# Optimization experiments

Measured on AMD Instinct MI355X. Metric: run time of the kernel, lower is better.

Reference implementation:

```python
import jax, jax.numpy as jnp
import numpy as np
from jax import lax

B, V, K, E = 32768, 256, 4, 2048
INTERVENTION_STRENGTH = 1.0
PROP_SCALE = 0.1
N_ROUNDS = 3


def setup_inputs() -> dict:
    key = jax.random.key(0)
    ks = jax.random.split(key, 20)
    s = 0.02
    return {
        "original_data": jax.random.normal(ks[0], (B, V), jnp.float32),
        "intervention_values": jax.random.normal(ks[1], (B, K), jnp.float32),
        "strengths": jax.random.uniform(ks[2], (E,), jnp.float32),
        "intervention_variables": jnp.arange(K, dtype=jnp.int32),
        "cause_idx": jax.random.randint(ks[3], (E,), 0, V, jnp.int32),
        "effect_idx": jax.random.randint(ks[4], (E,), 0, V, jnp.int32),
        # per-intervention-variable estimator MLPs: Linear(V,64) -> ReLU -> Linear(64,V)
        "est_W1": jax.random.normal(ks[5], (K, 64, V), jnp.float32) * s,
        "est_b1": jnp.zeros((K, 64), jnp.float32),
        "est_W2": jax.random.normal(ks[6], (K, V, 64), jnp.float32) * s,
        "est_b2": jnp.zeros((K, V), jnp.float32),
        # plausibility scorer: Linear(3V,128) -> ReLU -> Linear(128,64) -> ReLU -> Linear(64,1) -> Sigmoid
        "pl_W1": jax.random.normal(ks[7], (128, 3 * V), jnp.float32) * s,
        "pl_b1": jnp.zeros((128,), jnp.float32),
        "pl_W2": jax.random.normal(ks[8], (64, 128), jnp.float32) * s,
        "pl_b2": jnp.zeros((64,), jnp.float32),
        "pl_W3": jax.random.normal(ks[9], (1, 64), jnp.float32) * s,
        "pl_b3": jnp.zeros((1,), jnp.float32),
    }


def _propagate(data, cause_idx, effect_idx, strengths):
    # Faithful sequential in-place edge updates (effect of edge k may feed edge k+1).
    def step(d, ces):
        c, e, st = ces
        infl = d[:, c] * (st * PROP_SCALE)  # [B]
        return d.at[:, e].add(infl), None

    def round_body(d, _):
        d, _ = lax.scan(step, d, (cause_idx, effect_idx, strengths))
        return d, None

    d, _ = lax.scan(round_body, data, None, length=N_ROUNDS)
    return d


def reference(original_data, intervention_values, strengths,
              est_W1, est_b1, est_W2, est_b2,
              pl_W1, pl_b1, pl_W2, pl_b2, pl_W3, pl_b3,
              intervention_variables, cause_idx, effect_idx):
    x = original_data  # [B, V]
    ivars = intervention_variables  # [K] int, constant

    # do-intervention: overwrite selected columns
    intervened = x.at[:, ivars].set(intervention_values)  # [B, V]

    # intervention effect estimators, vectorized over the K intervened variables
    h = jax.nn.relu(jnp.einsum('bv,kov->bko', x, est_W1) + est_b1)          # [B, K, 64]
    eff = jnp.einsum('bko,kvo->bkv', h, est_W2) + est_b2                     # [B, K, V]
    mag = jnp.abs(intervention_values - x[:, ivars])                         # [B, K]
    intervention_effects = jnp.einsum('bkv,bk->bv', eff, mag) * INTERVENTION_STRENGTH  # [B, V]

    # sequential causal propagation over edge list, 3 rounds
    final_cf = _propagate(intervened + intervention_effects, cause_idx, effect_idx, strengths)

    # plausibility scorer MLP
    pin = jnp.concatenate([x, intervened, final_cf], axis=1)                 # [B, 3V]
    p = jax.nn.relu(pin @ pl_W1.T + pl_b1)
    p = jax.nn.relu(p @ pl_W2.T + pl_b2)
    plaus = jax.nn.sigmoid(p @ pl_W3.T + pl_b3)                              # [B, 1]

    impact = jnp.linalg.norm(final_cf - x, axis=1, keepdims=True)            # [B, 1]
    return final_cf, intervention_effects, plaus, impact
```

## Files before the change

kernel.cpp:

```cpp
#include <hip/hip_runtime.h>

#define BDIM 32768
#define VDIM 256
#define KVAR 4
#define EDIM 2048
#define SEGS 16
#define SEGLEN 128

typedef __attribute__((ext_vector_type(8))) short short8;
typedef __attribute__((ext_vector_type(4))) float f32x4;

__device__ __forceinline__ unsigned short f2b(float f){
  union { float f; unsigned u; } v; v.f = f;
  unsigned r = v.u + 0x7FFFu + ((v.u >> 16) & 1u);
  return (unsigned short)(r >> 16);
}
__device__ __forceinline__ float b2f(unsigned short h){
  union { unsigned u; float f; } v; v.u = ((unsigned)h) << 16;
  return v.f;
}
__device__ __forceinline__ short8 ldb8(const unsigned short* p){
  return *(const short8*)p;
}

__device__ __forceinline__ void gl_lds16(const unsigned short* g, unsigned short* l){
  __builtin_amdgcn_global_load_lds(
      (const __attribute__((address_space(1))) unsigned int*)g,
      (__attribute__((address_space(3))) unsigned int*)l, 16, 0, 0);
}

__device__ __forceinline__ void stage256(const unsigned short* Bt, int kB,
                                         int w, int lane, unsigned short* Bs){
#pragma unroll
  for (int i = 0; i < 4; i++){
    int g8 = i*8 + w;
    int r  = g8*8 + (lane >> 3);
    int s  = lane & 7;
    gl_lds16(Bt + (size_t)r*VDIM + kB + ((s ^ (r & 7)) << 3),
             Bs + (size_t)g8*512);
  }
}
__device__ __forceinline__ void stage128(const unsigned short* Bt, int kB,
                                         int w, int lane, unsigned short* Bs){
#pragma unroll
  for (int i = 0; i < 2; i++){
    int g8 = i*8 + w;
    int r  = g8*8 + (lane >> 3);
    int s  = lane & 7;
    gl_lds16(Bt + (size_t)r*VDIM + kB + ((s ^ (r & 7)) << 3),
             Bs + (size_t)g8*512);
  }
}
__device__ __forceinline__ void stageA64(const unsigned short* XBg, int rowBlk,
                                         int w, int lane, unsigned short* As){
#pragma unroll
  for (int i = 0; i < 4; i++){
    int pair = i*8 + w;
    int r = pair*2 + (lane >> 5);
    int s = lane & 31;
    gl_lds16(XBg + (size_t)(rowBlk + r)*VDIM + ((s ^ (r & 7)) << 3),
             As + (size_t)pair*512);
  }
}

__device__ __forceinline__ short8 bs_frag(const unsigned short* Bs, int c, int klocal){
  int slot = klocal >> 3;
  return *(const short8*)&Bs[(size_t)c*64 + ((slot ^ (c & 7)) << 3)];
}

template<int NF>
__device__ __forceinline__ void mm_lA(const unsigned short* Alds,
                                      const unsigned short* Bs,
                                      int rl0, int c0, int kb, int kB,
                                      f32x4 (&acc)[2][NF])
{
  int sw = (rl0 & 7) << 3;
#pragma unroll
  for (int k = 0; k < 2; k++){
    int ka = kB + k*32 + kb;
    short8 a0 = *(const short8*)&Alds[(size_t)rl0 * 256 + (ka ^ sw)];
    short8 a1 = *(const short8*)&Alds[(size_t)(rl0+16) * 256 + (ka ^ sw)];
#pragma unroll
    for (int fn = 0; fn < NF; fn++){
      short8 b = bs_frag(Bs, c0 + fn*16, k*32 + kb);
      acc[0][fn] = __builtin_amdgcn_mfma_f32_16x16x32_bf16(a0, b, acc[0][fn], 0, 0, 0);
      acc[1][fn] = __builtin_amdgcn_mfma_f32_16x16x32_bf16(a1, b, acc[1][fn], 0, 0, 0);
    }
  }
}
template<int NF, int KSZ>
__device__ __forceinline__ void mm_l1(const unsigned short* Alds, int ldaE,
                                      const unsigned short* Bt, int ldb,
                                      int rl0, int c0, int kb,
                                      f32x4 (&acc)[NF])
{
  int sw = (rl0 & 7) << 3;
#pragma unroll
  for (int k0 = 0; k0 < KSZ; k0 += 32){
    int ka = k0 + kb;
    short8 a0 = *(const short8*)&Alds[(size_t)rl0 * ldaE + (ka ^ sw)];
#pragma unroll
    for (int fn = 0; fn < NF; fn++){
      short8 b = ldb8(Bt + (size_t)(c0 + fn*16)*ldb + ka);
      acc[fn] = __builtin_amdgcn_mfma_f32_16x16x32_bf16(a0, b, acc[fn], 0, 0, 0);
    }
  }
}

__global__ __launch_bounds__(256) void prep_seg(
    const float* X, const float* IV, const int* ivars,
    const float* eW1, const float* eW2, const float* pW1, const float* pW2,
    const int* cidx, const int* eidx, const float* stren,
    unsigned short* XB,
    unsigned short* bt1, unsigned short* bt2,
    unsigned short* w1ab, unsigned short* w1c,
    unsigned short* w2bf, float* w1bcol, int* colmap,
    float* delta, float* segs)
{
  if (blockIdx.x < 1024){
    __shared__ int lc[SEGLEN];
    __shared__ int le[SEGLEN];
    __shared__ float la[SEGLEN];
    int bid = blockIdx.x;
    int seg = bid >> 6;
    int rowbase = (bid & 63) * 4;
    int w = threadIdx.x >> 6, lane = threadIdx.x & 63;
    int row = rowbase + w;
    int k0 = seg * SEGLEN;
    for (int t = threadIdx.x; t < SEGLEN; t += 256){
      lc[t] = cidx[k0 + t]; le[t] = eidx[k0 + t]; la[t] = stren[k0 + t] * 0.1f;
    }
    __syncthreads();
    float r0 = (row == lane)        ? 1.f : 0.f;
    float r1 = (row == lane + 64)   ? 1.f : 0.f;
    float r2 = (row == lane + 128)  ? 1.f : 0.f;
    float r3 = (row == lane + 192)  ? 1.f : 0.f;
    for (int t = 0; t < SEGLEN; t++){
      int cs = __builtin_amdgcn_readfirstlane(lc[t]);
      int es = __builtin_amdgcn_readfirstlane(le[t]);
      float a = la[t];
      float vr;
      switch (cs >> 6){ case 0: vr = r0; break; case 1: vr = r1; break;
                        case 2: vr = r2; break; default: vr = r3; }
      float v = __shfl(vr, cs & 63, 64);
      float add = (lane == (es & 63)) ? a * v : 0.f;
      switch (es >> 6){ case 0: r0 += add; break; case 1: r1 += add; break;
                        case 2: r2 += add; break; default: r3 += add; }
    }
    float* out = segs + (size_t)seg * 65536 + (size_t)row * 256;
    out[lane] = r0; out[lane + 64] = r1; out[lane + 128] = r2; out[lane + 192] = r3;
    return;
  }
  int stride = 1024 * 256;
  int g0 = (blockIdx.x - 1024) * 256 + threadIdx.x;
  for (int i = g0; i < (BDIM * VDIM) / 8; i += stride){
    const float* p = X + (size_t)i * 8;
    f32x4 lo = *(const f32x4*)p;
    f32x4 hi = *(const f32x4*)(p + 4);
    short8 r;
    r[0]=(short)f2b(lo[0]); r[1]=(short)f2b(lo[1]); r[2]=(short)f2b(lo[2]); r[3]=(short)f2b(lo[3]);
    r[4]=(short)f2b(hi[0]); r[5]=(short)f2b(hi[1]); r[6]=(short)f2b(hi[2]); r[7]=(short)f2b(hi[3]);
    *(short8*)(XB + (size_t)i * 8) = r;
  }
  for (int i = g0; i < 65536; i += stride) bt1[i] = f2b(eW1[i]);
  for (int i = g0; i < 65536; i += stride){
    int v = i >> 8, r = i & 255;
    bt2[i] = f2b(eW2[(r >> 6) * 16384 + v * 64 + (r & 63)]);
  }
  for (int i = g0; i < 32768; i += stride){
    int o = i >> 8, v = i & 255;
    w1ab[i] = f2b(pW1[o*768 + v] + pW1[o*768 + 256 + v]);
    w1c[i]  = f2b(pW1[o*768 + 512 + v]);
  }
  for (int i = g0; i < 8192; i += stride) w2bf[i] = f2b(pW2[i]);
  for (int i = g0; i < 512; i += stride){
    int o = i >> 2, k = i & 3;
    w1bcol[i] = pW1[o*768 + 256 + ivars[k]];
  }
  for (int i = g0; i < VDIM; i += stride){
    int m = -1;
#pragma unroll
    for (int k = 0; k < KVAR; k++) if (ivars[k] == i) m = k;
    colmap[i] = m;
  }
  for (int i = g0; i < BDIM * KVAR; i += stride){
    int b = i >> 2, k = i & 3;
    delta[i] = IV[i] - X[(size_t)b * VDIM + ivars[k]];
  }
}

__global__ __launch_bounds__(256) void combine4(const float* S, float* Out)
{
  int m = blockIdx.x >> 6;
  int rb = (blockIdx.x & 63) * 4;
  int c = threadIdx.x;
  __shared__ float v[4][256];
  const float* base = S + (size_t)m * 4 * 65536;
#pragma unroll
  for (int r = 0; r < 4; r++) v[r][c] = base[(size_t)(rb + r) * 256 + c];
  __syncthreads();
  for (int p = 1; p < 4; p++){
    const float* Bm = base + (size_t)p * 65536;
    float a0 = 0.f, a1 = 0.f, a2 = 0.f, a3 = 0.f;
    for (int k = 0; k < 256; k += 4){
      f32x4 v0 = *(const f32x4*)&v[0][k];
      f32x4 v1 = *(const f32x4*)&v[1][k];
      f32x4 v2 = *(const f32x4*)&v[2][k];
      f32x4 v3 = *(const f32x4*)&v[3][k];
#pragma unroll
      for (int j = 0; j < 4; j++){
        float bk = Bm[(size_t)(k + j) * 256 + c];
        a0 += v0[j] * bk; a1 += v1[j] * bk; a2 += v2[j] * bk; a3 += v3[j] * bk;
      }
    }
    __syncthreads();
    v[0][c] = a0; v[1][c] = a1; v[2][c] = a2; v[3][c] = a3;
    __syncthreads();
  }
#pragma unroll
  for (int r = 0; r < 4; r++) Out[(size_t)m * 65536 + (size_t)(rb + r) * 256 + c] = v[r][c];
}

__global__ __launch_bounds__(256) void powM(const float* R, unsigned short* Mt)
{
  int rb = blockIdx.x * 4;
  int c = threadIdx.x;
  __shared__ float v[4][256];
#pragma unroll
  for (int r = 0; r < 4; r++) v[r][c] = R[(size_t)(rb + r) * 256 + c];
  __syncthreads();
  for (int p = 0; p < 2; p++){
    float a0 = 0.f, a1 = 0.f, a2 = 0.f, a3 = 0.f;
    for (int k = 0; k < 256; k += 4){
      f32x4 v0 = *(const f32x4*)&v[0][k];
      f32x4 v1 = *(const f32x4*)&v[1][k];
      f32x4 v2 = *(const f32x4*)&v[2][k];
      f32x4 v3 = *(const f32x4*)&v[3][k];
#pragma unroll
      for (int j = 0; j < 4; j++){
        float bk = R[(size_t)(k + j) * 256 + c];
        a0 += v0[j] * bk; a1 += v1[j] * bk; a2 += v2[j] * bk; a3 += v3[j] * bk;
      }
    }
    __syncthreads();
    v[0][c] = a0; v[1][c] = a1; v[2][c] = a2; v[3][c] = a3;
    __syncthreads();
  }
#pragma unroll
  for (int r = 0; r < 4; r++) Mt[(size_t)c * 256 + (rb + r)] = f2b(v[r][c]);
}

__global__ __launch_bounds__(512) void mega3(
    const float* IV, const unsigned short* XB,
    const unsigned short* Bt1, const unsigned short* Bt2, const unsigned short* Mt,
    const unsigned short* W1ab, const unsigned short* W1c, const unsigned short* W2bf,
    const float* eb1, const float* eb2, const float* delta, const int* colmap,
    const float* w1bcol, const float* pb1, const float* pb2,
    const float* W3, const float* pb3,
    float* effOut, float* outF, float* plausOut, float* impOut)
{
  __shared__ unsigned short xbs[64 * 256];
  __shared__ unsigned short buf[64 * 256];
  __shared__ unsigned short Bs0[256 * 64];
  __shared__ unsigned short Bs1[256 * 64];
  __shared__ float impLds[64 * 4];
  int tid = threadIdx.x, w = tid >> 6, lane = tid & 63;
  int rowg = w >> 2, colg = w & 3;
  int rowBlk = blockIdx.x * 64;
  int rl0 = rowg * 32 + (lane & 15);
  int colBase = colg * 64;
  int c0 = colBase + (lane & 15);
  int kb = (lane >> 4) * 8;
  f32x4 acc[2][4];

  auto stage_unit = [&](int u, unsigned short* Bs){
    if (u < 4)       stage256(Bt1, u*64, w, lane, Bs);
    else if (u < 8)  stage256(Bt2, (u-4)*64, w, lane, Bs);
    else if (u < 12) stage256(Mt, (u-8)*64, w, lane, Bs);
    else           { stage128(W1ab, (u-12)*64, w, lane, Bs);
                     stage128(W1c,  (u-12)*64, w, lane, Bs + 8192); }
  };

  stageA64(XB, rowBlk, w, lane, xbs);
  stage_unit(0, Bs0);
  __syncthreads();

#pragma unroll
  for (int fm = 0; fm < 2; fm++)
#pragma unroll
    for (int fn = 0; fn < 4; fn++) acc[fm][fn] = (f32x4){0.f,0.f,0.f,0.f};
#pragma unroll
  for (int kc = 0; kc < 4; kc++){
    int u = kc;
    stage_unit(u + 1, (u & 1) ? Bs0 : Bs1);
    __builtin_amdgcn_s_setprio(1);
    mm_lA<4>(xbs, (u & 1) ? Bs1 : Bs0, rl0, c0, kb, kc*64, acc);
    __builtin_amdgcn_s_setprio(0);
    __syncthreads();
  }
  {
    float b1v[4];
#pragma unroll
    for (int fn = 0; fn < 4; fn++) b1v[fn] = eb1[colBase + fn*16 + (lane & 15)];
#pragma unroll
    for (int fm = 0; fm < 2; fm++)
#pragma unroll
      for (int i = 0; i < 4; i++){
        int rl = rowg*32 + fm*16 + (lane >> 4)*4 + i;
        int gr = rowBlk + rl;
        float mg = fabsf(delta[gr*4 + colg]);
        int sw = (rl & 7) << 3;
#pragma unroll
        for (int fn = 0; fn < 4; fn++){
          int col = colBase + fn*16 + (lane & 15);
          float h = acc[fm][fn][i] + b1v[fn];
          h = h > 0.f ? h : 0.f;
          buf[(size_t)rl*256 + (col ^ sw)] = f2b(h * mg);
        }
      }
  }
  __syncthreads();

#pragma unroll
  for (int fm = 0; fm < 2; fm++)
#pragma unroll
    for (int fn = 0; fn < 4; fn++) acc[fm][fn] = (f32x4){0.f,0.f,0.f,0.f};
#pragma unroll
  for (int kc = 0; kc < 4; kc++){
    int u = 4 + kc;
    stage_unit(u + 1, (u & 1) ? Bs0 : Bs1);
    __builtin_amdgcn_s_setprio(1);
    mm_lA<4>(buf, (u & 1) ? Bs1 : Bs0, rl0, c0, kb, kc*64, acc);
    __builtin_amdgcn_s_setprio(0);
    __syncthreads();
  }
  {
    float bb0[4], bb1[4], bb2[4], bb3[4];
    int imv[4];
#pragma unroll
    for (int fn = 0; fn < 4; fn++){
      int col = colBase + fn*16 + (lane & 15);
      bb0[fn] = eb2[col]; bb1[fn] = eb2[256 + col];
      bb2[fn] = eb2[512 + col]; bb3[fn] = eb2[768 + col];
      imv[fn] = colmap[col];
    }
#pragma unroll
    for (int fm = 0; fm < 2; fm++)
#pragma unroll
      for (int i = 0; i < 4; i++){
        int rl = rowg*32 + fm*16 + (lane >> 4)*4 + i;
        int gr = rowBlk + rl;
        f32x4 dl = *(const f32x4*)&delta[gr*4];
        float d0a = fabsf(dl[0]), d1a = fabsf(dl[1]), d2a = fabsf(dl[2]), d3a = fabsf(dl[3]);
        int sw = (rl & 7) << 3;
#pragma unroll
        for (int fn = 0; fn < 4; fn++){
          int col = colBase + fn*16 + (lane & 15);
          float eff = acc[fm][fn][i] + d0a*bb0[fn] + d1a*bb1[fn] + d2a*bb2[fn] + d3a*bb3[fn];
          size_t idx = (size_t)gr*VDIM + col;
          effOut[idx] = eff;
          float base = (imv[fn] >= 0) ? IV[gr*4 + imv[fn]]
                                      : b2f(xbs[(size_t)rl*256 + (col ^ sw)]);
          buf[(size_t)rl*256 + (col ^ sw)] = f2b(base + eff);
        }
      }
  }
  __syncthreads();

#pragma unroll
  for (int fm = 0; fm < 2; fm++)
#pragma unroll
    for (int fn = 0; fn < 4; fn++) acc[fm][fn] = (f32x4){0.f,0.f,0.f,0.f};
#pragma unroll
  for (int kc = 0; kc < 4; kc++){
    int u = 8 + kc;
    stage_unit(u + 1, (u & 1) ? Bs0 : Bs1);
    __builtin_amdgcn_s_setprio(1);
    mm_lA<4>(buf, (u & 1) ? Bs1 : Bs0, rl0, c0, kb, kc*64, acc);
    __builtin_amdgcn_s_setprio(0);
    __syncthreads();
  }
  {
#pragma unroll
    for (int fm = 0; fm < 2; fm++)
#pragma unroll
      for (int i = 0; i < 4; i++){
        int rl = rowg*32 + fm*16 + (lane >> 4)*4 + i;
        int gr = rowBlk + rl;
        int sw = (rl & 7) << 3;
        float ss = 0.f;
#pragma unroll
        for (int fn = 0; fn < 4; fn++){
          int col = colBase + fn*16 + (lane & 15);
          size_t idx = (size_t)gr*VDIM + col;
          float fv = acc[fm][fn][i];
          outF[idx] = fv;
          buf[(size_t)rl*256 + (col ^ sw)] = f2b(fv);
          float d = fv - b2f(xbs[(size_t)rl*256 + (col ^ sw)]);
          ss += d * d;
        }
        ss += __shfl_xor(ss, 1, 64); ss += __shfl_xor(ss, 2, 64);
        ss += __shfl_xor(ss, 4, 64); ss += __shfl_xor(ss, 8, 64);
        if ((lane & 15) == 0) impLds[rl*4 + colg] = ss;
      }
  }
  __syncthreads();

  {
    f32x4 a4[2][2];
#pragma unroll
    for (int fm = 0; fm < 2; fm++)
#pragma unroll
      for (int fn = 0; fn < 2; fn++) a4[fm][fn] = (f32x4){0.f,0.f,0.f,0.f};
    int c4 = colg * 32 + (lane & 15);
#pragma unroll
    for (int kc = 0; kc < 4; kc++){
      int u = 12 + kc;
      if (kc < 3) stage_unit(u + 1, (u & 1) ? Bs0 : Bs1);
      const unsigned short* B = (u & 1) ? Bs1 : Bs0;
      __builtin_amdgcn_s_setprio(1);
      mm_lA<2>(xbs, B, rl0, c4, kb, kc*64, a4);
      mm_lA<2>(buf, B + 8192, rl0, c4, kb, kc*64, a4);
      __builtin_amdgcn_s_setprio(0);
      __syncthreads();
    }
    float bv[2];
    f32x4 wb[2];
#pragma unroll
    for (int fn = 0; fn < 2; fn++){
      int col = colg*32 + fn*16 + (lane & 15);
      bv[fn] = pb1[col];
      wb[fn] = *(const f32x4*)&w1bcol[col*4];
    }
#pragma unroll
    for (int fm = 0; fm < 2; fm++)
#pragma unroll
      for (int i = 0; i < 4; i++){
        int rl = rowg*32 + fm*16 + (lane >> 4)*4 + i;
        int gr = rowBlk + rl;
        f32x4 dl = *(const f32x4*)&delta[gr*4];
        int sw = (rl & 7) << 3;
#pragma unroll
        for (int fn = 0; fn < 2; fn++){
          int col = colg*32 + fn*16 + (lane & 15);
          float p = a4[fm][fn][i] + bv[fn]
                  + dl[0]*wb[fn][0] + dl[1]*wb[fn][1] + dl[2]*wb[fn][2] + dl[3]*wb[fn][3];
          p = p > 0.f ? p : 0.f;
          buf[(size_t)rl*128 + (col ^ sw)] = f2b(p);
        }
      }
  }
  __syncthreads();

  if (w < 4){
    int rl0b = w * 16 + (lane & 15);
    f32x4 a2[4];
#pragma unroll
    for (int fn = 0; fn < 4; fn++) a2[fn] = (f32x4){0.f,0.f,0.f,0.f};
    mm_l1<4, 128>(buf, 128, W2bf, 128, rl0b, (lane & 15), kb, a2);
    float b2v[4], w3v[4];
#pragma unroll
    for (int fn = 0; fn < 4; fn++){
      int col = fn*16 + (lane & 15);
      b2v[fn] = pb2[col]; w3v[fn] = W3[col];
    }
    float b3v = pb3[0];
#pragma unroll
    for (int i = 0; i < 4; i++){
      float s = 0.f;
#pragma unroll
      for (int fn = 0; fn < 4; fn++){
        float p2 = a2[fn][i] + b2v[fn];
        p2 = p2 > 0.f ? p2 : 0.f;
        s += p2 * w3v[fn];
      }
      s += __shfl_xor(s, 1, 64); s += __shfl_xor(s, 2, 64);
      s += __shfl_xor(s, 4, 64); s += __shfl_xor(s, 8, 64);
      if ((lane & 15) == 0){
        int gr = rowBlk + w*16 + (lane >> 4)*4 + i;
        plausOut[gr] = 1.f / (1.f + expf(-(s + b3v)));
      }
    }
  } else if (w == 4){
    f32x4 v = *(const f32x4*)&impLds[lane * 4];
    impOut[rowBlk + lane] = sqrtf(v[0] + v[1] + v[2] + v[3]);
  }
}

#define WS_XB     ((size_t)0)
#define WS_DELTA  ((size_t)16777216)
#define WS_SEG    ((size_t)17301504)
#define WS_T2     ((size_t)21495808)
#define WS_R      ((size_t)22544384)
#define WS_MT     ((size_t)22806528)
#define WS_BT1    ((size_t)22937600)
#define WS_BT2    ((size_t)23068672)
#define WS_W1AB   ((size_t)23199744)
#define WS_W1C    ((size_t)23265280)
#define WS_W2BF   ((size_t)23330816)
#define WS_W1BCOL ((size_t)23347200)
#define WS_COLMAP ((size_t)23349248)

extern "C" void kernel_launch(void* const* d_in, const int* in_sizes, int n_in,
                              void* d_out, int out_size, void* d_ws, size_t ws_size,
                              hipStream_t stream)
{
  const float* X     = (const float*)d_in[0];
  const float* IV    = (const float*)d_in[1];
  const float* STR   = (const float*)d_in[2];
  const int*   IVARS = (const int*)d_in[3];
  const int*   CIDX  = (const int*)d_in[4];
  const int*   EIDX  = (const int*)d_in[5];
  const float* EW1   = (const float*)d_in[6];
  const float* EB1   = (const float*)d_in[7];
  const float* EW2   = (const float*)d_in[8];
  const float* EB2   = (const float*)d_in[9];
  const float* PW1   = (const float*)d_in[10];
  const float* PB1   = (const float*)d_in[11];
  const float* PW2   = (const float*)d_in[12];
  const float* PB2   = (const float*)d_in[13];
  const float* PW3   = (const float*)d_in[14];
  const float* PB3   = (const float*)d_in[15];

  char* ws = (char*)d_ws;
  unsigned short* XB     = (unsigned short*)(ws + WS_XB);
  float*          DELTA  = (float*)(ws + WS_DELTA);
  float*          SEG    = (float*)(ws + WS_SEG);
  float*          T2     = (float*)(ws + WS_T2);
  float*          Rm     = (float*)(ws + WS_R);
  unsigned short* MT     = (unsigned short*)(ws + WS_MT);
  unsigned short* BT1    = (unsigned short*)(ws + WS_BT1);
  unsigned short* BT2    = (unsigned short*)(ws + WS_BT2);
  unsigned short* W1AB   = (unsigned short*)(ws + WS_W1AB);
  unsigned short* W1C    = (unsigned short*)(ws + WS_W1C);
  unsigned short* W2BF   = (unsigned short*)(ws + WS_W2BF);
  float*          W1BCOL = (float*)(ws + WS_W1BCOL);
  int*            COLMAP = (int*)(ws + WS_COLMAP);

  float* outF   = (float*)d_out;
  float* outEff = outF + (size_t)BDIM * VDIM;
  float* outPl  = outEff + (size_t)BDIM * VDIM;
  float* outIm  = outPl + BDIM;

  prep_seg<<<2048, 256, 0, stream>>>(X, IV, IVARS, EW1, EW2, PW1, PW2,
                                     CIDX, EIDX, STR,
                                     XB, BT1, BT2, W1AB, W1C, W2BF, W1BCOL, COLMAP,
                                     DELTA, SEG);
  combine4<<<256, 256, 0, stream>>>(SEG, T2);
  combine4<<<64, 256, 0, stream>>>(T2, Rm);
  powM<<<64, 256, 0, stream>>>(Rm, MT);

  mega3<<<512, 512, 0, stream>>>(IV, XB, BT1, BT2, MT, W1AB, W1C, W2BF,
                                 EB1, EB2, DELTA, COLMAP, W1BCOL,
                                 PB1, PB2, PW3, PB3,
                                 outEff, outF, outPl, outIm);

  (void)in_sizes; (void)n_in; (void)out_size; (void)ws_size;
}
```

Measured before the change: 167.6 us.

## Double waves per block in fused kernel and widen matrix-combine grids

```diff
diff --git a/kernel.cpp b/kernel.cpp
--- a/kernel.cpp
+++ b/kernel.cpp
@@ -32,8 +32,8 @@
 __device__ __forceinline__ void stage256(const unsigned short* Bt, int kB,
                                          int w, int lane, unsigned short* Bs){
 #pragma unroll
-  for (int i = 0; i < 4; i++){
-    int g8 = i*8 + w;
+  for (int i = 0; i < 2; i++){
+    int g8 = i*16 + w;
     int r  = g8*8 + (lane >> 3);
     int s  = lane & 7;
     gl_lds16(Bt + (size_t)r*VDIM + kB + ((s ^ (r & 7)) << 3),
@@ -42,20 +42,17 @@
 }
 __device__ __forceinline__ void stage128(const unsigned short* Bt, int kB,
                                          int w, int lane, unsigned short* Bs){
-#pragma unroll
-  for (int i = 0; i < 2; i++){
-    int g8 = i*8 + w;
-    int r  = g8*8 + (lane >> 3);
-    int s  = lane & 7;
-    gl_lds16(Bt + (size_t)r*VDIM + kB + ((s ^ (r & 7)) << 3),
-             Bs + (size_t)g8*512);
-  }
+  int g8 = w;
+  int r  = g8*8 + (lane >> 3);
+  int s  = lane & 7;
+  gl_lds16(Bt + (size_t)r*VDIM + kB + ((s ^ (r & 7)) << 3),
+           Bs + (size_t)g8*512);
 }
 __device__ __forceinline__ void stageA64(const unsigned short* XBg, int rowBlk,
                                          int w, int lane, unsigned short* As){
 #pragma unroll
-  for (int i = 0; i < 4; i++){
-    int pair = i*8 + w;
+  for (int i = 0; i < 2; i++){
+    int pair = i*16 + w;
     int r = pair*2 + (lane >> 5);
     int s = lane & 31;
     gl_lds16(XBg + (size_t)(rowBlk + r)*VDIM + ((s ^ (r & 7)) << 3),
@@ -189,68 +186,52 @@
   }
 }
 
-__global__ __launch_bounds__(256) void combine4(const float* S, float* Out)
-{
-  int m = blockIdx.x >> 6;
-  int rb = (blockIdx.x & 63) * 4;
+__global__ __launch_bounds__(256) void combine4w(const float* S, float* Out)
+{
+  int m = blockIdx.x >> 8;
+  int r = blockIdx.x & 255;
   int c = threadIdx.x;
-  __shared__ float v[4][256];
+  __shared__ float v[256];
   const float* base = S + (size_t)m * 4 * 65536;
-#pragma unroll
-  for (int r = 0; r < 4; r++) v[r][c] = base[(size_t)(rb + r) * 256 + c];
+  v[c] = base[(size_t)r * 256 + c];
   __syncthreads();
   for (int p = 1; p < 4; p++){
     const float* Bm = base + (size_t)p * 65536;
-    float a0 = 0.f, a1 = 0.f, a2 = 0.f, a3 = 0.f;
-    for (int k = 0; k < 256; k += 4){
-      f32x4 v0 = *(const f32x4*)&v[0][k];
-      f32x4 v1 = *(const f32x4*)&v[1][k];
-      f32x4 v2 = *(const f32x4*)&v[2][k];
-      f32x4 v3 = *(const f32x4*)&v[3][k];
-#pragma unroll
-      for (int j = 0; j < 4; j++){
-        float bk = Bm[(size_t)(k + j) * 256 + c];
-        a0 += v0[j] * bk; a1 += v1[j] * bk; a2 += v2[j] * bk; a3 += v3[j] * bk;
-      }
-    }
-    __syncthreads();
-    v[0][c] = a0; v[1][c] = a1; v[2][c] = a2; v[3][c] = a3;
-    __syncthreads();
-  }
-#pragma unroll
-  for (int r = 0; r < 4; r++) Out[(size_t)m * 65536 + (size_t)(rb + r) * 256 + c] = v[r][c];
-}
-
-__global__ __launch_bounds__(256) void powM(const float* R, unsigned short* Mt)
-{
-  int rb = blockIdx.x * 4;
+    float a = 0.f;
+    for (int k = 0; k < 256; k += 8){
+#pragma unroll
+      for (int j = 0; j < 8; j++)
+        a += v[k + j] * Bm[(size_t)(k + j) * 256 + c];
+    }
+    __syncthreads();
+    v[c] = a;
+    __syncthreads();
+  }
+  Out[(size_t)m * 65536 + (size_t)r * 256 + c] = v[c];
+}
+
+__global__ __launch_bounds__(256) void powMw(const float* R, unsigned short* Mt)
+{
+  int r = blockIdx.x;
   int c = threadIdx.x;
-  __shared__ float v[4][256];
-#pragma unroll
-  for (int r = 0; r < 4; r++) v[r][c] = R[(size_t)(rb + r) * 256 + c];
+  __shared__ float v[256];
+  v[c] = R[(size_t)r * 256 + c];
   __syncthreads();
   for (int p = 0; p < 2; p++){
-    float a0 = 0.f, a1 = 0.f, a2 = 0.f, a3 = 0.f;
-    for (int k = 0; k < 256; k += 4){
-      f32x4 v0 = *(const f32x4*)&v[0][k];
-      f32x4 v1 = *(const f32x4*)&v[1][k];
-      f32x4 v2 = *(const f32x4*)&v[2][k];
-      f32x4 v3 = *(const f32x4*)&v[3][k];
-#pragma unroll
-      for (int j = 0; j < 4; j++){
-        float bk = R[(size_t)(k + j) * 256 + c];
-        a0 += v0[j] * bk; a1 += v1[j] * bk; a2 += v2[j] * bk; a3 += v3[j] * bk;
-      }
-    }
-    __syncthreads();
-    v[0][c] = a0; v[1][c] = a1; v[2][c] = a2; v[3][c] = a3;
-    __syncthreads();
-  }
-#pragma unroll
-  for (int r = 0; r < 4; r++) Mt[(size_t)c * 256 + (rb + r)] = f2b(v[r][c]);
-}
-
-__global__ __launch_bounds__(512) void mega3(
+    float a = 0.f;
+    for (int k = 0; k < 256; k += 8){
+#pragma unroll
+      for (int j = 0; j < 8; j++)
+        a += v[k + j] * R[(size_t)(k + j) * 256 + c];
+    }
+    __syncthreads();
+    v[c] = a;
+    __syncthreads();
+  }
+  Mt[(size_t)c * 256 + r] = f2b(v[c]);
+}
+
+__global__ __launch_bounds__(1024) void mega3(
     const float* IV, const unsigned short* XB,
     const unsigned short* Bt1, const unsigned short* Bt2, const unsigned short* Mt,
     const unsigned short* W1ab, const unsigned short* W1c, const unsigned short* W2bf,
@@ -263,15 +244,15 @@
   __shared__ unsigned short buf[64 * 256];
   __shared__ unsigned short Bs0[256 * 64];
   __shared__ unsigned short Bs1[256 * 64];
-  __shared__ float impLds[64 * 4];
+  __shared__ float impLds[64 * 8];
   int tid = threadIdx.x, w = tid >> 6, lane = tid & 63;
-  int rowg = w >> 2, colg = w & 3;
+  int rowg = w >> 3, colg = w & 7;
   int rowBlk = blockIdx.x * 64;
   int rl0 = rowg * 32 + (lane & 15);
-  int colBase = colg * 64;
+  int colBase = colg * 32;
   int c0 = colBase + (lane & 15);
   int kb = (lane >> 4) * 8;
-  f32x4 acc[2][4];
+  f32x4 acc[2][2];
 
   auto stage_unit = [&](int u, unsigned short* Bs){
     if (u < 4)       stage256(Bt1, u*64, w, lane, Bs);
@@ -288,30 +269,31 @@
 #pragma unroll
   for (int fm = 0; fm < 2; fm++)
 #pragma unroll
-    for (int fn = 0; fn < 4; fn++) acc[fm][fn] = (f32x4){0.f,0.f,0.f,0.f};
+    for (int fn = 0; fn < 2; fn++) acc[fm][fn] = (f32x4){0.f,0.f,0.f,0.f};
 #pragma unroll
   for (int kc = 0; kc < 4; kc++){
     int u = kc;
     stage_unit(u + 1, (u & 1) ? Bs0 : Bs1);
     __builtin_amdgcn_s_setprio(1);
-    mm_lA<4>(xbs, (u & 1) ? Bs1 : Bs0, rl0, c0, kb, kc*64, acc);
+    mm_lA<2>(xbs, (u & 1) ? Bs1 : Bs0, rl0, c0, kb, kc*64, acc);
     __builtin_amdgcn_s_setprio(0);
     __syncthreads();
   }
   {
-    float b1v[4];
-#pragma unroll
-    for (int fn = 0; fn < 4; fn++) b1v[fn] = eb1[colBase + fn*16 + (lane & 15)];
+    float b1v[2];
+#pragma unroll
+    for (int fn = 0; fn < 2; fn++) b1v[fn] = eb1[colBase + fn*16 + (lane & 15)];
+    int kI = colg >> 1;
 #pragma unroll
     for (int fm = 0; fm < 2; fm++)
 #pragma unroll
       for (int i = 0; i < 4; i++){
         int rl = rowg*32 + fm*16 + (lane >> 4)*4 + i;
         int gr = rowBlk + rl;
-        float mg = fabsf(delta[gr*4 + colg]);
+        float mg = fabsf(delta[gr*4 + kI]);
         int sw = (rl & 7) << 3;
 #pragma unroll
-        for (int fn = 0; fn < 4; fn++){
+        for (int fn = 0; fn < 2; fn++){
           int col = colBase + fn*16 + (lane & 15);
           float h = acc[fm][fn][i] + b1v[fn];
           h = h > 0.f ? h : 0.f;
@@ -324,21 +306,21 @@
 #pragma unroll
   for (int fm = 0; fm < 2; fm++)
 #pragma unroll
-    for (int fn = 0; fn < 4; fn++) acc[fm][fn] = (f32x4){0.f,0.f,0.f,0.f};
+    for (int fn = 0; fn < 2; fn++) acc[fm][fn] = (f32x4){0.f,0.f,0.f,0.f};
 #pragma unroll
   for (int kc = 0; kc < 4; kc++){
     int u = 4 + kc;
     stage_unit(u + 1, (u & 1) ? Bs0 : Bs1);
     __builtin_amdgcn_s_setprio(1);
-    mm_lA<4>(buf, (u & 1) ? Bs1 : Bs0, rl0, c0, kb, kc*64, acc);
+    mm_lA<2>(buf, (u & 1) ? Bs1 : Bs0, rl0, c0, kb, kc*64, acc);
     __builtin_amdgcn_s_setprio(0);
     __syncthreads();
   }
   {
-    float bb0[4], bb1[4], bb2[4], bb3[4];
-    int imv[4];
-#pragma unroll
-    for (int fn = 0; fn < 4; fn++){
+    float bb0[2], bb1[2], bb2[2], bb3[2];
+    int imv[2];
+#pragma unroll
+    for (int fn = 0; fn < 2; fn++){
       int col = colBase + fn*16 + (lane & 15);
       bb0[fn] = eb2[col]; bb1[fn] = eb2[256 + col];
       bb2[fn] = eb2[512 + col]; bb3[fn] = eb2[768 + col];
@@ -354,7 +336,7 @@
         float d0a = fabsf(dl[0]), d1a = fabsf(dl[1]), d2a = fabsf(dl[2]), d3a = fabsf(dl[3]);
         int sw = (rl & 7) << 3;
 #pragma unroll
-        for (int fn = 0; fn < 4; fn++){
+        for (int fn = 0; fn < 2; fn++){
           int col = colBase + fn*16 + (lane & 15);
           float eff = acc[fm][fn][i] + d0a*bb0[fn] + d1a*bb1[fn] + d2a*bb2[fn] + d3a*bb3[fn];
           size_t idx = (size_t)gr*VDIM + col;
@@ -370,13 +352,13 @@
 #pragma unroll
   for (int fm = 0; fm < 2; fm++)
 #pragma unroll
-    for (int fn = 0; fn < 4; fn++) acc[fm][fn] = (f32x4){0.f,0.f,0.f,0.f};
+    for (int fn = 0; fn < 2; fn++) acc[fm][fn] = (f32x4){0.f,0.f,0.f,0.f};
 #pragma unroll
   for (int kc = 0; kc < 4; kc++){
     int u = 8 + kc;
     stage_unit(u + 1, (u & 1) ? Bs0 : Bs1);
     __builtin_amdgcn_s_setprio(1);
-    mm_lA<4>(buf, (u & 1) ? Bs1 : Bs0, rl0, c0, kb, kc*64, acc);
+    mm_lA<2>(buf, (u & 1) ? Bs1 : Bs0, rl0, c0, kb, kc*64, acc);
     __builtin_amdgcn_s_setprio(0);
     __syncthreads();
   }
@@ -390,7 +372,7 @@
         int sw = (rl & 7) << 3;
         float ss = 0.f;
 #pragma unroll
-        for (int fn = 0; fn < 4; fn++){
+        for (int fn = 0; fn < 2; fn++){
           int col = colBase + fn*16 + (lane & 15);
           size_t idx = (size_t)gr*VDIM + col;
           float fv = acc[fm][fn][i];
@@ -401,37 +383,29 @@
         }
         ss += __shfl_xor(ss, 1, 64); ss += __shfl_xor(ss, 2, 64);
         ss += __shfl_xor(ss, 4, 64); ss += __shfl_xor(ss, 8, 64);
-        if ((lane & 15) == 0) impLds[rl*4 + colg] = ss;
+        if ((lane & 15) == 0) impLds[rl*8 + colg] = ss;
       }
   }
   __syncthreads();
 
   {
-    f32x4 a4[2][2];
-#pragma unroll
-    for (int fm = 0; fm < 2; fm++)
-#pragma unroll
-      for (int fn = 0; fn < 2; fn++) a4[fm][fn] = (f32x4){0.f,0.f,0.f,0.f};
-    int c4 = colg * 32 + (lane & 15);
+    f32x4 a4[2][1];
+#pragma unroll
+    for (int fm = 0; fm < 2; fm++) a4[fm][0] = (f32x4){0.f,0.f,0.f,0.f};
+    int c4 = colg*16 + (lane & 15);
 #pragma unroll
     for (int kc = 0; kc < 4; kc++){
       int u = 12 + kc;
       if (kc < 3) stage_unit(u + 1, (u & 1) ? Bs0 : Bs1);
       const unsigned short* B = (u & 1) ? Bs1 : Bs0;
       __builtin_amdgcn_s_setprio(1);
-      mm_lA<2>(xbs, B, rl0, c4, kb, kc*64, a4);
-      mm_lA<2>(buf, B + 8192, rl0, c4, kb, kc*64, a4);
+      mm_lA<1>(xbs, B, rl0, c4, kb, kc*64, a4);
+      mm_lA<1>(buf, B + 8192, rl0, c4, kb, kc*64, a4);
       __builtin_amdgcn_s_setprio(0);
       __syncthreads();
     }
-    float bv[2];
-    f32x4 wb[2];
-#pragma unroll
-    for (int fn = 0; fn < 2; fn++){
-      int col = colg*32 + fn*16 + (lane & 15);
-      bv[fn] = pb1[col];
-      wb[fn] = *(const f32x4*)&w1bcol[col*4];
-    }
+    float bv = pb1[c4];
+    f32x4 wb = *(const f32x4*)&w1bcol[c4*4];
 #pragma unroll
     for (int fm = 0; fm < 2; fm++)
 #pragma unroll
@@ -440,14 +414,10 @@
         int gr = rowBlk + rl;
         f32x4 dl = *(const f32x4*)&delta[gr*4];
         int sw = (rl & 7) << 3;
-#pragma unroll
-        for (int fn = 0; fn < 2; fn++){
-          int col = colg*32 + fn*16 + (lane & 15);
-          float p = a4[fm][fn][i] + bv[fn]
-                  + dl[0]*wb[fn][0] + dl[1]*wb[fn][1] + dl[2]*wb[fn][2] + dl[3]*wb[fn][3];
-          p = p > 0.f ? p : 0.f;
-          buf[(size_t)rl*128 + (col ^ sw)] = f2b(p);
-        }
+        float p = a4[fm][0][i] + bv
+                + dl[0]*wb[0] + dl[1]*wb[1] + dl[2]*wb[2] + dl[3]*wb[3];
+        p = p > 0.f ? p : 0.f;
+        buf[(size_t)rl*128 + (c4 ^ sw)] = f2b(p);
       }
   }
   __syncthreads();
@@ -482,8 +452,9 @@
       }
     }
   } else if (w == 4){
-    f32x4 v = *(const f32x4*)&impLds[lane * 4];
-    impOut[rowBlk + lane] = sqrtf(v[0] + v[1] + v[2] + v[3]);
+    f32x4 v0 = *(const f32x4*)&impLds[lane * 8];
+    f32x4 v1 = *(const f32x4*)&impLds[lane * 8 + 4];
+    impOut[rowBlk + lane] = sqrtf(v0[0]+v0[1]+v0[2]+v0[3]+v1[0]+v1[1]+v1[2]+v1[3]);
   }
 }
 
@@ -546,14 +517,14 @@
                                      CIDX, EIDX, STR,
                                      XB, BT1, BT2, W1AB, W1C, W2BF, W1BCOL, COLMAP,
                                      DELTA, SEG);
-  combine4<<<256, 256, 0, stream>>>(SEG, T2);
-  combine4<<<64, 256, 0, stream>>>(T2, Rm);
-  powM<<<64, 256, 0, stream>>>(Rm, MT);
-
-  mega3<<<512, 512, 0, stream>>>(IV, XB, BT1, BT2, MT, W1AB, W1C, W2BF,
-                                 EB1, EB2, DELTA, COLMAP, W1BCOL,
-                                 PB1, PB2, PW3, PB3,
-                                 outEff, outF, outPl, outIm);
+  combine4w<<<1024, 256, 0, stream>>>(SEG, T2);
+  combine4w<<<256, 256, 0, stream>>>(T2, Rm);
+  powMw<<<256, 256, 0, stream>>>(Rm, MT);
+
+  mega3<<<512, 1024, 0, stream>>>(IV, XB, BT1, BT2, MT, W1AB, W1C, W2BF,
+                                  EB1, EB2, DELTA, COLMAP, W1BCOL,
+                                  PB1, PB2, PW3, PB3,
+                                  outEff, outF, outPl, outIm);
 
   (void)in_sizes; (void)n_in; (void)out_size; (void)ws_size;
 }
```

New measurement: 247.6 us. +47.7%, slower.

## Move activation tiles from LDS to global scratch to cut shared memory use

Applied to the files above, without the earlier changes.

```diff
diff --git a/kernel.cpp b/kernel.cpp
--- a/kernel.cpp
+++ b/kernel.cpp
@@ -51,17 +51,6 @@
              Bs + (size_t)g8*512);
   }
 }
-__device__ __forceinline__ void stageA64(const unsigned short* XBg, int rowBlk,
-                                         int w, int lane, unsigned short* As){
-#pragma unroll
-  for (int i = 0; i < 4; i++){
-    int pair = i*8 + w;
-    int r = pair*2 + (lane >> 5);
-    int s = lane & 31;
-    gl_lds16(XBg + (size_t)(rowBlk + r)*VDIM + ((s ^ (r & 7)) << 3),
-             As + (size_t)pair*512);
-  }
-}
 
 __device__ __forceinline__ short8 bs_frag(const unsigned short* Bs, int c, int klocal){
   int slot = klocal >> 3;
@@ -69,17 +58,16 @@
 }
 
 template<int NF>
-__device__ __forceinline__ void mm_lA(const unsigned short* Alds,
+__device__ __forceinline__ void mm_gA(const unsigned short* A, int lda, int r0,
                                       const unsigned short* Bs,
-                                      int rl0, int c0, int kb, int kB,
+                                      int c0, int kb, int kB,
                                       f32x4 (&acc)[2][NF])
 {
-  int sw = (rl0 & 7) << 3;
 #pragma unroll
   for (int k = 0; k < 2; k++){
     int ka = kB + k*32 + kb;
-    short8 a0 = *(const short8*)&Alds[(size_t)rl0 * 256 + (ka ^ sw)];
-    short8 a1 = *(const short8*)&Alds[(size_t)(rl0+16) * 256 + (ka ^ sw)];
+    short8 a0 = ldb8(A + (size_t)r0*lda + ka);
+    short8 a1 = ldb8(A + (size_t)(r0+16)*lda + ka);
 #pragma unroll
     for (int fn = 0; fn < NF; fn++){
       short8 b = bs_frag(Bs, c0 + fn*16, k*32 + kb);
@@ -89,16 +77,15 @@
   }
 }
 template<int NF, int KSZ>
-__device__ __forceinline__ void mm_l1(const unsigned short* Alds, int ldaE,
+__device__ __forceinline__ void mm_g1(const unsigned short* A, int lda,
                                       const unsigned short* Bt, int ldb,
-                                      int rl0, int c0, int kb,
+                                      int r0g, int c0, int kb,
                                       f32x4 (&acc)[NF])
 {
-  int sw = (rl0 & 7) << 3;
 #pragma unroll
   for (int k0 = 0; k0 < KSZ; k0 += 32){
     int ka = k0 + kb;
-    short8 a0 = *(const short8*)&Alds[(size_t)rl0 * ldaE + (ka ^ sw)];
+    short8 a0 = ldb8(A + (size_t)r0g*lda + ka);
 #pragma unroll
     for (int fn = 0; fn < NF; fn++){
       short8 b = ldb8(Bt + (size_t)(c0 + fn*16)*ldb + ka);
@@ -250,17 +237,16 @@
   for (int r = 0; r < 4; r++) Mt[(size_t)c * 256 + (rb + r)] = f2b(v[r][c]);
 }
 
-__global__ __launch_bounds__(512) void mega3(
+__global__ __launch_bounds__(512) void mega4(
     const float* IV, const unsigned short* XB,
     const unsigned short* Bt1, const unsigned short* Bt2, const unsigned short* Mt,
     const unsigned short* W1ab, const unsigned short* W1c, const unsigned short* W2bf,
     const float* eb1, const float* eb2, const float* delta, const int* colmap,
     const float* w1bcol, const float* pb1, const float* pb2,
     const float* W3, const float* pb3,
+    unsigned short* scrH, unsigned short* scrD,
     float* effOut, float* outF, float* plausOut, float* impOut)
 {
-  __shared__ unsigned short xbs[64 * 256];
-  __shared__ unsigned short buf[64 * 256];
   __shared__ unsigned short Bs0[256 * 64];
   __shared__ unsigned short Bs1[256 * 64];
   __shared__ float impLds[64 * 4];
@@ -268,10 +254,12 @@
   int rowg = w >> 2, colg = w & 3;
   int rowBlk = blockIdx.x * 64;
   int rl0 = rowg * 32 + (lane & 15);
+  int r0 = rowBlk + rl0;
   int colBase = colg * 64;
   int c0 = colBase + (lane & 15);
   int kb = (lane >> 4) * 8;
   f32x4 acc[2][4];
+  unsigned short xcap[2][4][4];
 
   auto stage_unit = [&](int u, unsigned short* Bs){
     if (u < 4)       stage256(Bt1, u*64, w, lane, Bs);
@@ -281,8 +269,16 @@
                      stage128(W1c,  (u-12)*64, w, lane, Bs + 8192); }
   };
 
-  stageA64(XB, rowBlk, w, lane, xbs);
   stage_unit(0, Bs0);
+#pragma unroll
+  for (int fm = 0; fm < 2; fm++)
+#pragma unroll
+    for (int i = 0; i < 4; i++){
+      int gr = rowBlk + rowg*32 + fm*16 + (lane >> 4)*4 + i;
+#pragma unroll
+      for (int fn = 0; fn < 4; fn++)
+        xcap[fm][i][fn] = XB[(size_t)gr*VDIM + colBase + fn*16 + (lane & 15)];
+    }
   __syncthreads();
 
 #pragma unroll
@@ -294,7 +290,7 @@
     int u = kc;
     stage_unit(u + 1, (u & 1) ? Bs0 : Bs1);
     __builtin_amdgcn_s_setprio(1);
-    mm_lA<4>(xbs, (u & 1) ? Bs1 : Bs0, rl0, c0, kb, kc*64, acc);
+    mm_gA<4>(XB, VDIM, r0, (u & 1) ? Bs1 : Bs0, c0, kb, kc*64, acc);
     __builtin_amdgcn_s_setprio(0);
     __syncthreads();
   }
@@ -306,16 +302,14 @@
     for (int fm = 0; fm < 2; fm++)
 #pragma unroll
       for (int i = 0; i < 4; i++){
-        int rl = rowg*32 + fm*16 + (lane >> 4)*4 + i;
-        int gr = rowBlk + rl;
+        int gr = rowBlk + rowg*32 + fm*16 + (lane >> 4)*4 + i;
         float mg = fabsf(delta[gr*4 + colg]);
-        int sw = (rl & 7) << 3;
 #pragma unroll
         for (int fn = 0; fn < 4; fn++){
           int col = colBase + fn*16 + (lane & 15);
           float h = acc[fm][fn][i] + b1v[fn];
           h = h > 0.f ? h : 0.f;
-          buf[(size_t)rl*256 + (col ^ sw)] = f2b(h * mg);
+          scrH[(size_t)gr*VDIM + col] = f2b(h * mg);
         }
       }
   }
@@ -330,7 +324,7 @@
     int u = 4 + kc;
     stage_unit(u + 1, (u & 1) ? Bs0 : Bs1);
     __builtin_amdgcn_s_setprio(1);
-    mm_lA<4>(buf, (u & 1) ? Bs1 : Bs0, rl0, c0, kb, kc*64, acc);
+    mm_gA<4>(scrH, VDIM, r0, (u & 1) ? Bs1 : Bs0, c0, kb, kc*64, acc);
     __builtin_amdgcn_s_setprio(0);
     __syncthreads();
   }
@@ -348,20 +342,17 @@
     for (int fm = 0; fm < 2; fm++)
 #pragma unroll
       for (int i = 0; i < 4; i++){
-        int rl = rowg*32 + fm*16 + (lane >> 4)*4 + i;
-        int gr = rowBlk + rl;
+        int gr = rowBlk + rowg*32 + fm*16 + (lane >> 4)*4 + i;
         f32x4 dl = *(const f32x4*)&delta[gr*4];
         float d0a = fabsf(dl[0]), d1a = fabsf(dl[1]), d2a = fabsf(dl[2]), d3a = fabsf(dl[3]);
-        int sw = (rl & 7) << 3;
 #pragma unroll
         for (int fn = 0; fn < 4; fn++){
           int col = colBase + fn*16 + (lane & 15);
           float eff = acc[fm][fn][i] + d0a*bb0[fn] + d1a*bb1[fn] + d2a*bb2[fn] + d3a*bb3[fn];
           size_t idx = (size_t)gr*VDIM + col;
           effOut[idx] = eff;
-          float base = (imv[fn] >= 0) ? IV[gr*4 + imv[fn]]
-                                      : b2f(xbs[(size_t)rl*256 + (col ^ sw)]);
-          buf[(size_t)rl*256 + (col ^ sw)] = f2b(base + eff);
+          float base = (imv[fn] >= 0) ? IV[gr*4 + imv[fn]] : b2f(xcap[fm][i][fn]);
+          scrD[idx] = f2b(base + eff);
         }
       }
   }
@@ -376,7 +367,7 @@
     int u = 8 + kc;
     stage_unit(u + 1, (u & 1) ? Bs0 : Bs1);
     __builtin_amdgcn_s_setprio(1);
-    mm_lA<4>(buf, (u & 1) ? Bs1 : Bs0, rl0, c0, kb, kc*64, acc);
+    mm_gA<4>(scrD, VDIM, r0, (u & 1) ? Bs1 : Bs0, c0, kb, kc*64, acc);
     __builtin_amdgcn_s_setprio(0);
     __syncthreads();
   }
@@ -387,7 +378,6 @@
       for (int i = 0; i < 4; i++){
         int rl = rowg*32 + fm*16 + (lane >> 4)*4 + i;
         int gr = rowBlk + rl;
-        int sw = (rl & 7) << 3;
         float ss = 0.f;
 #pragma unroll
         for (int fn = 0; fn < 4; fn++){
@@ -395,8 +385,8 @@
           size_t idx = (size_t)gr*VDIM + col;
           float fv = acc[fm][fn][i];
           outF[idx] = fv;
-          buf[(size_t)rl*256 + (col ^ sw)] = f2b(fv);
-          float d = fv - b2f(xbs[(size_t)rl*256 + (col ^ sw)]);
+          scrH[idx] = f2b(fv);
+          float d = fv - b2f(xcap[fm][i][fn]);
           ss += d * d;
         }
         ss += __shfl_xor(ss, 1, 64); ss += __shfl_xor(ss, 2, 64);
@@ -419,8 +409,8 @@
       if (kc < 3) stage_unit(u + 1, (u & 1) ? Bs0 : Bs1);
       const unsigned short* B = (u & 1) ? Bs1 : Bs0;
       __builtin_amdgcn_s_setprio(1);
-      mm_lA<2>(xbs, B, rl0, c4, kb, kc*64, a4);
-      mm_lA<2>(buf, B + 8192, rl0, c4, kb, kc*64, a4);
+      mm_gA<2>(XB,   VDIM, r0, B,        c4, kb, kc*64, a4);
+      mm_gA<2>(scrH, VDIM, r0, B + 8192, c4, kb, kc*64, a4);
       __builtin_amdgcn_s_setprio(0);
       __syncthreads();
     }
@@ -436,28 +426,26 @@
     for (int fm = 0; fm < 2; fm++)
 #pragma unroll
       for (int i = 0; i < 4; i++){
-        int rl = rowg*32 + fm*16 + (lane >> 4)*4 + i;
-        int gr = rowBlk + rl;
+        int gr = rowBlk + rowg*32 + fm*16 + (lane >> 4)*4 + i;
         f32x4 dl = *(const f32x4*)&delta[gr*4];
-        int sw = (rl & 7) << 3;
 #pragma unroll
         for (int fn = 0; fn < 2; fn++){
           int col = colg*32 + fn*16 + (lane & 15);
           float p = a4[fm][fn][i] + bv[fn]
                   + dl[0]*wb[fn][0] + dl[1]*wb[fn][1] + dl[2]*wb[fn][2] + dl[3]*wb[fn][3];
           p = p > 0.f ? p : 0.f;
-          buf[(size_t)rl*128 + (col ^ sw)] = f2b(p);
+          scrD[(size_t)gr*128 + col] = f2b(p);
         }
       }
   }
   __syncthreads();
 
   if (w < 4){
-    int rl0b = w * 16 + (lane & 15);
+    int r0g = rowBlk + w*16 + (lane & 15);
     f32x4 a2[4];
 #pragma unroll
     for (int fn = 0; fn < 4; fn++) a2[fn] = (f32x4){0.f,0.f,0.f,0.f};
-    mm_l1<4, 128>(buf, 128, W2bf, 128, rl0b, (lane & 15), kb, a2);
+    mm_g1<4, 128>(scrD, 128, W2bf, 128, r0g, (lane & 15), kb, a2);
     float b2v[4], w3v[4];
 #pragma unroll
     for (int fn = 0; fn < 4; fn++){
@@ -500,6 +488,9 @@
 #define WS_W2BF   ((size_t)23330816)
 #define WS_W1BCOL ((size_t)23347200)
 #define WS_COLMAP ((size_t)23349248)
+#define WS_HS     ((size_t)25165824)
+#define WS_DB     ((size_t)41943040)
+#define WS_NEED   ((size_t)58720256)
 
 extern "C" void kernel_launch(void* const* d_in, const int* in_sizes, int n_in,
                               void* d_out, int out_size, void* d_ws, size_t ws_size,
@@ -536,6 +527,8 @@
   unsigned short* W2BF   = (unsigned short*)(ws + WS_W2BF);
   float*          W1BCOL = (float*)(ws + WS_W1BCOL);
   int*            COLMAP = (int*)(ws + WS_COLMAP);
+  unsigned short* SCRH   = (unsigned short*)(ws + WS_HS);
+  unsigned short* SCRD   = (unsigned short*)(ws + WS_DB);
 
   float* outF   = (float*)d_out;
   float* outEff = outF + (size_t)BDIM * VDIM;
@@ -550,9 +543,9 @@
   combine4<<<64, 256, 0, stream>>>(T2, Rm);
   powM<<<64, 256, 0, stream>>>(Rm, MT);
 
-  mega3<<<512, 512, 0, stream>>>(IV, XB, BT1, BT2, MT, W1AB, W1C, W2BF,
+  mega4<<<512, 512, 0, stream>>>(IV, XB, BT1, BT2, MT, W1AB, W1C, W2BF,
                                  EB1, EB2, DELTA, COLMAP, W1BCOL,
-                                 PB1, PB2, PW3, PB3,
+                                 PB1, PB2, PW3, PB3, SCRH, SCRD,
                                  outEff, outF, outPl, outIm);
 
   (void)in_sizes; (void)n_in; (void)out_size; (void)ws_size;
```

After: 209.6 us. 1.25x slower.
